# Optimization experiments

Measured on AMD Instinct MI355X. Metric: run time of the kernel, lower is better.

The kernel has to match this reference:

```python
import jax, jax.numpy as jnp
import numpy as np

B, S, C, H, W = 4, 8, 3, 384, 384
K = 5
CK = C * K


def conv1x1(x, w, b):
    # x: [B, Cin, H, W], w: [Cout, Cin], b: [Cout] -> [B, Cout, H, W]
    return jnp.einsum('bchw,oc->bohw', x, w) + b[None, :, None, None]


def mlp(x, w1, b1, w2, b2):
    return conv1x1(jax.nn.relu(conv1x1(x, w1, b1)), w2, b2)


def gaussian_density(x, mu_k, sigma):
    # x: [B,C,H,W], mu_k: [B,K,C,H,W], sigma: [B,K,H,W] -> density [B,K,H,W]
    s2 = sigma * sigma
    dist = jnp.sum((x[:, None] - mu_k) ** 2, axis=2)  # [B,K,H,W]
    return (2.0 * np.pi * s2) ** (-C / 2.0) * jnp.exp(-dist / (2.0 * s2))


def gmm_block(params, x, pi, mu, sigma):
    b = x.shape[0]
    mu_k = mu.reshape(b, K, C, H, W)
    dens = gaussian_density(x, mu_k, sigma)          # [B,K,H,W] (computed once, reused)
    alpha = pi * dens                                 # [B,K,H,W]
    rho = alpha * dens                                # [B,K,H,W]
    pi_new = jax.nn.softmax(mlp(jnp.concatenate([pi, alpha], 1), *params['pi']), axis=1)
    mu_new = jax.nn.sigmoid(mlp(jnp.concatenate([x, mu, rho], 1), *params['mu']))
    sigma_new = jnp.exp(jax.nn.relu(mlp(jnp.concatenate([x, mu_new, rho], 1), *params['sigma'])))
    dens2 = gaussian_density(x, mu_new.reshape(b, K, C, H, W), sigma_new)
    gamma = jax.nn.sigmoid(mlp(pi_new * dens2, *params['gamma']))  # [B,1,H,W]
    return pi_new, mu_new, sigma_new, gamma


def setup_inputs() -> dict:
    key = jax.random.key(0)
    ks = jax.random.split(key, 20)
    frames = jax.random.uniform(ks[0], (B, S, C, H, W), jnp.float32)
    targets = jax.random.uniform(ks[1], (B, S, C, H, W), jnp.float32)
    mu0 = jax.random.randint(ks[2], (B, CK, H, W), 0, 255).astype(jnp.float32) / 255.0
    def wb(k1, k2, cout, cin):
        return (jax.random.normal(k1, (cout, cin), jnp.float32) * 0.1,
                jax.random.normal(k2, (cout,), jnp.float32) * 0.1)
    pi_w1, pi_b1 = wb(ks[3], ks[4], K, 2 * K)
    pi_w2, pi_b2 = wb(ks[5], ks[6], K, K)
    mu_w1, mu_b1 = wb(ks[7], ks[8], CK, C + CK + K)
    mu_w2, mu_b2 = wb(ks[9], ks[10], CK, CK)
    sg_w1, sg_b1 = wb(ks[11], ks[12], K, C + CK + K)
    sg_w2, sg_b2 = wb(ks[13], ks[14], K, K)
    ga_w1, ga_b1 = wb(ks[15], ks[16], K, K)
    ga_w2, ga_b2 = wb(ks[17], ks[18], 1, K)
    return dict(frames=frames, targets=targets, mu0=mu0,
                pi_w1=pi_w1, pi_b1=pi_b1, pi_w2=pi_w2, pi_b2=pi_b2,
                mu_w1=mu_w1, mu_b1=mu_b1, mu_w2=mu_w2, mu_b2=mu_b2,
                sg_w1=sg_w1, sg_b1=sg_b1, sg_w2=sg_w2, sg_b2=sg_b2,
                ga_w1=ga_w1, ga_b1=ga_b1, ga_w2=ga_w2, ga_b2=ga_b2)


def reference(frames, targets, mu0,
              pi_w1, pi_b1, pi_w2, pi_b2,
              mu_w1, mu_b1, mu_w2, mu_b2,
              sg_w1, sg_b1, sg_w2, sg_b2,
              ga_w1, ga_b1, ga_w2, ga_b2):
    params = dict(pi=(pi_w1, pi_b1, pi_w2, pi_b2),
                  mu=(mu_w1, mu_b1, mu_w2, mu_b2),
                  sigma=(sg_w1, sg_b1, sg_w2, sg_b2),
                  gamma=(ga_w1, ga_b1, ga_w2, ga_b2))
    b = frames.shape[0]
    # init_gmm
    pi0 = jnp.ones((b, K, H, W), frames.dtype) / K
    sigma0 = jnp.ones((b, K, H, W), frames.dtype)

    def step(carry, frame):
        pi, mu, sigma = carry
        pi, mu, sigma, gamma = gmm_block(params, frame, pi, mu, sigma)
        return (pi, mu, sigma), gamma

    xs = jnp.moveaxis(frames, 1, 0)  # [S,B,C,H,W]
    _, gammas = jax.lax.scan(step, (pi0, mu0, sigma0), xs)
    return jnp.moveaxis(gammas, 0, 1)  # [B,S,1,H,W]
```

## Files before the change

### kernel.cpp

```cpp
#include <hip/hip_runtime.h>


namespace {

constexpr int Kk = 5;
constexpr int Cc = 3;
constexpr int CKc = 15;
constexpr int Bb = 4;
constexpr int Ss = 8;
constexpr int HWc = 384 * 384;

constexpr int PW1 = 0,   PP1 = 12;
constexpr int PB1 = 60;
constexpr int PW2 = 68,  PP2 = 8;
constexpr int PB2 = 108;
constexpr int MW1 = 116, MP1 = 24;
constexpr int MB1 = 476;
constexpr int MW2 = 492, MP2 = 16;
constexpr int MB2 = 732;
constexpr int SW1 = 748, SP1 = 24;
constexpr int SB1 = 868;
constexpr int SW2 = 876, SP2 = 8;
constexpr int SB2 = 916;
constexpr int GW1 = 924, GP1 = 8;
constexpr int GB1 = 964;
constexpr int GW2 = 972;
constexpr int GB2 = 980;
constexpr int WTOT = 984;

__device__ __forceinline__ float rcpf(float x) { return __builtin_amdgcn_rcpf(x); }
__device__ __forceinline__ float sigm(float x) { return rcpf(1.0f + __expf(-x)); }
__device__ __forceinline__ float relu(float x) { return fmaxf(x, 0.0f); }

__device__ __forceinline__ void stage(float* W, int dst, const float* __restrict__ src,
                                      int rows, int cols, int pitch, int tid) {
    for (int t = tid; t < rows * pitch; t += 256) {
        int r = t / pitch, c = t - r * pitch;
        W[dst + t] = (c < cols) ? src[r * cols + c] : 0.0f;
    }
}

__global__ __launch_bounds__(256) void gmm_seq_kernel(
    const float* __restrict__ frames,
    const float* __restrict__ mu0,
    const float* __restrict__ pw1, const float* __restrict__ pb1,
    const float* __restrict__ pw2, const float* __restrict__ pb2,
    const float* __restrict__ mw1, const float* __restrict__ mb1,
    const float* __restrict__ mw2, const float* __restrict__ mb2,
    const float* __restrict__ sw1, const float* __restrict__ sb1,
    const float* __restrict__ sw2, const float* __restrict__ sb2,
    const float* __restrict__ gw1, const float* __restrict__ gb1,
    const float* __restrict__ gw2, const float* __restrict__ gb2,
    float* __restrict__ out)
{
    __shared__ float sW[WTOT];
    {
        const int t = threadIdx.x;
        stage(sW, PW1, pw1, Kk, 2 * Kk, PP1, t);
        stage(sW, PB1, pb1, 1, Kk, 8, t);
        stage(sW, PW2, pw2, Kk, Kk, PP2, t);
        stage(sW, PB2, pb2, 1, Kk, 8, t);
        stage(sW, MW1, mw1, CKc, 23, MP1, t);
        stage(sW, MB1, mb1, 1, CKc, 16, t);
        stage(sW, MW2, mw2, CKc, CKc, MP2, t);
        stage(sW, MB2, mb2, 1, CKc, 16, t);
        stage(sW, SW1, sw1, Kk, 23, SP1, t);
        stage(sW, SB1, sb1, 1, Kk, 8, t);
        stage(sW, SW2, sw2, Kk, Kk, SP2, t);
        stage(sW, SB2, sb2, 1, Kk, 8, t);
        stage(sW, GW1, gw1, Kk, Kk, GP1, t);
        stage(sW, GB1, gb1, 1, Kk, 8, t);
        stage(sW, GW2, gw2, 1, Kk, 8, t);
        stage(sW, GB2, gb2, 1, 1, 4, t);
    }
    __syncthreads();

    const int tid = blockIdx.x * blockDim.x + threadIdx.x;
    const int b  = tid / HWc;
    const int hw = tid - b * HWc;

    const float C0 = 0.06349363593424097f;

    float pi[Kk], mu[CKc], rinv[Kk];
#pragma unroll
    for (int k = 0; k < Kk; k++) { pi[k] = 0.2f; rinv[k] = 1.0f; }
    {
        const float* mp = mu0 + (size_t)b * CKc * HWc + hw;
#pragma unroll
        for (int j = 0; j < CKc; j++) mu[j] = mp[(size_t)j * HWc];
    }

    const float* fbase = frames + ((size_t)b * Ss * Cc) * HWc + hw;
    float x[Cc];
#pragma unroll
    for (int c = 0; c < Cc; c++) x[c] = fbase[(size_t)c * HWc];

#pragma unroll 1
    for (int s = 0; s < Ss; s++) {
        unsigned woff = 0;
        asm volatile("" : "+v"(woff));
        woff &= ~3u;
#define LW(IDX) sW[woff + (IDX)]

        float xn[Cc];
        if (s + 1 < Ss) {
            const float* fp = fbase + ((size_t)(s + 1) * Cc) * HWc;
#pragma unroll
            for (int c = 0; c < Cc; c++) xn[c] = fp[(size_t)c * HWc];
        }

        float dens[Kk];
#pragma unroll
        for (int k = 0; k < Kk; k++) {
            float inv_s2 = rinv[k] * rinv[k];
            float d0 = x[0] - mu[k * Cc + 0];
            float d1 = x[1] - mu[k * Cc + 1];
            float d2 = x[2] - mu[k * Cc + 2];
            float dist = d0 * d0 + d1 * d1 + d2 * d2;
            float coef = C0 * inv_s2 * rinv[k];
            dens[k] = coef * __expf(-0.5f * dist * inv_s2);
        }

        float alpha[Kk], rho[Kk];
#pragma unroll
        for (int k = 0; k < Kk; k++) { alpha[k] = pi[k] * dens[k]; rho[k] = alpha[k] * dens[k]; }

        float piN[Kk];
        {
            float in[2 * Kk];
#pragma unroll
            for (int k = 0; k < Kk; k++) { in[k] = pi[k]; in[Kk + k] = alpha[k]; }
            float h[Kk];
#pragma unroll
            for (int j = 0; j < Kk; j++) {
                float a = LW(PB1 + j);
#pragma unroll
                for (int i = 0; i < 2 * Kk; i++) a = fmaf(LW(PW1 + j * PP1 + i), in[i], a);
                h[j] = relu(a);
            }
            float o[Kk];
            float m = -1e30f;
#pragma unroll
            for (int j = 0; j < Kk; j++) {
                float a = LW(PB2 + j);
#pragma unroll
                for (int i = 0; i < Kk; i++) a = fmaf(LW(PW2 + j * PP2 + i), h[i], a);
                o[j] = a; m = fmaxf(m, a);
            }
            float sum = 0.0f;
#pragma unroll
            for (int j = 0; j < Kk; j++) { o[j] = __expf(o[j] - m); sum += o[j]; }
            float r = rcpf(sum);
#pragma unroll
            for (int j = 0; j < Kk; j++) piN[j] = o[j] * r;
        }

        float in23[23];
        in23[0] = x[0]; in23[1] = x[1]; in23[2] = x[2];
#pragma unroll
        for (int j = 0; j < CKc; j++) in23[3 + j] = mu[j];
#pragma unroll
        for (int k = 0; k < Kk; k++) in23[18 + k] = rho[k];

        float muN[CKc];
        {
            float h[CKc];
#pragma unroll
            for (int j = 0; j < CKc; j++) {
                float a = LW(MB1 + j);
#pragma unroll
                for (int i = 0; i < 23; i++) a = fmaf(LW(MW1 + j * MP1 + i), in23[i], a);
                h[j] = relu(a);
            }
#pragma unroll
            for (int j = 0; j < CKc; j++) {
                float a = LW(MB2 + j);
#pragma unroll
                for (int i = 0; i < CKc; i++) a = fmaf(LW(MW2 + j * MP2 + i), h[i], a);
                muN[j] = sigm(a);
            }
        }

#pragma unroll
        for (int j = 0; j < CKc; j++) in23[3 + j] = muN[j];
        float rinvN[Kk];
        {
            float h[Kk];
#pragma unroll
            for (int j = 0; j < Kk; j++) {
                float a = LW(SB1 + j);
#pragma unroll
                for (int i = 0; i < 23; i++) a = fmaf(LW(SW1 + j * SP1 + i), in23[i], a);
                h[j] = relu(a);
            }
#pragma unroll
            for (int j = 0; j < Kk; j++) {
                float a = LW(SB2 + j);
#pragma unroll
                for (int i = 0; i < Kk; i++) a = fmaf(LW(SW2 + j * SP2 + i), h[i], a);
                rinvN[j] = __expf(-relu(a));
            }
        }

        float gin[Kk];
#pragma unroll
        for (int k = 0; k < Kk; k++) {
            float inv_s2 = rinvN[k] * rinvN[k];
            float d0 = x[0] - muN[k * Cc + 0];
            float d1 = x[1] - muN[k * Cc + 1];
            float d2 = x[2] - muN[k * Cc + 2];
            float dist = d0 * d0 + d1 * d1 + d2 * d2;
            float coef = C0 * inv_s2 * rinvN[k];
            gin[k] = piN[k] * (coef * __expf(-0.5f * dist * inv_s2));
        }
        {
            float h[Kk];
#pragma unroll
            for (int j = 0; j < Kk; j++) {
                float a = LW(GB1 + j);
#pragma unroll
                for (int i = 0; i < Kk; i++) a = fmaf(LW(GW1 + j * GP1 + i), gin[i], a);
                h[j] = relu(a);
            }
            float go = LW(GB2);
#pragma unroll
            for (int i = 0; i < Kk; i++) go = fmaf(LW(GW2 + i), h[i], go);
            out[(size_t)(b * Ss + s) * HWc + hw] = sigm(go);
        }
#undef LW

#pragma unroll
        for (int k = 0; k < Kk; k++) { pi[k] = piN[k]; rinv[k] = rinvN[k]; }
#pragma unroll
        for (int j = 0; j < CKc; j++) mu[j] = muN[j];
#pragma unroll
        for (int c = 0; c < Cc; c++) x[c] = xn[c];
    }
}

}

extern "C" void kernel_launch(void* const* d_in, const int* in_sizes, int n_in,
                              void* d_out, int out_size, void* d_ws, size_t ws_size,
                              hipStream_t stream) {
    const float* frames = (const float*)d_in[0];
    const float* mu0    = (const float*)d_in[2];
    const float* pw1 = (const float*)d_in[3];
    const float* pb1 = (const float*)d_in[4];
    const float* pw2 = (const float*)d_in[5];
    const float* pb2 = (const float*)d_in[6];
    const float* mw1 = (const float*)d_in[7];
    const float* mb1 = (const float*)d_in[8];
    const float* mw2 = (const float*)d_in[9];
    const float* mb2 = (const float*)d_in[10];
    const float* sw1 = (const float*)d_in[11];
    const float* sb1 = (const float*)d_in[12];
    const float* sw2 = (const float*)d_in[13];
    const float* sb2 = (const float*)d_in[14];
    const float* gw1 = (const float*)d_in[15];
    const float* gb1 = (const float*)d_in[16];
    const float* gw2 = (const float*)d_in[17];
    const float* gb2 = (const float*)d_in[18];
    float* out = (float*)d_out;

    const int total = Bb * HWc;
    const int block = 256;
    const int grid = (total + block - 1) / block;

    gmm_seq_kernel<<<grid, block, 0, stream>>>(
        frames, mu0,
        pw1, pb1, pw2, pb2,
        mw1, mb1, mw2, mb2,
        sw1, sb1, sw2, sb2,
        gw1, gb1, gw2, gb2,
        out);
}
```

Measured before the change: 336.5 us.

## Process two pixels per thread with float2 packed math

New measurement: 315.9 us. 6.1% less time.

```diff
diff --git a/kernel.cpp b/kernel.cpp
--- a/kernel.cpp
+++ b/kernel.cpp
@@ -9,6 +9,9 @@
 constexpr int Bb = 4;
 constexpr int Ss = 8;
 constexpr int HWc = 384 * 384;
+constexpr int HW2 = HWc / 2;
+
+typedef float v2f __attribute__((ext_vector_type(2)));
 
 constexpr int PW1 = 0,   PP1 = 12;
 constexpr int PB1 = 60;
@@ -29,8 +32,15 @@
 constexpr int WTOT = 984;
 
 __device__ __forceinline__ float rcpf(float x) { return __builtin_amdgcn_rcpf(x); }
-__device__ __forceinline__ float sigm(float x) { return rcpf(1.0f + __expf(-x)); }
-__device__ __forceinline__ float relu(float x) { return fmaxf(x, 0.0f); }
+
+__device__ __forceinline__ v2f vsplat(float w) { v2f r = {w, w}; return r; }
+__device__ __forceinline__ v2f vfma(v2f a, v2f b, v2f c) { return __builtin_elementwise_fma(a, b, c); }
+__device__ __forceinline__ v2f wfma(float w, v2f x, v2f c) { return vfma(vsplat(w), x, c); }
+__device__ __forceinline__ v2f vexp(v2f v) { v2f r; r.x = __expf(v.x); r.y = __expf(v.y); return r; }
+__device__ __forceinline__ v2f vrcp(v2f v) { v2f r; r.x = rcpf(v.x); r.y = rcpf(v.y); return r; }
+__device__ __forceinline__ v2f vmax(v2f a, v2f b) { return __builtin_elementwise_max(a, b); }
+__device__ __forceinline__ v2f vrelu(v2f a) { return vmax(a, vsplat(0.0f)); }
+__device__ __forceinline__ v2f vsigm(v2f a) { return vrcp(vsplat(1.0f) + vexp(-a)); }
 
 __device__ __forceinline__ void stage(float* W, int dst, const float* __restrict__ src,
                                       int rows, int cols, int pitch, int tid) {
@@ -75,25 +85,27 @@
     }
     __syncthreads();
 
-    const int tid = blockIdx.x * blockDim.x + threadIdx.x;
-    const int b  = tid / HWc;
-    const int hw = tid - b * HWc;
+    const int t2 = blockIdx.x * blockDim.x + threadIdx.x;
+    const int b   = t2 / HW2;
+    const int rem = t2 - b * HW2;
 
     const float C0 = 0.06349363593424097f;
 
-    float pi[Kk], mu[CKc], rinv[Kk];
-#pragma unroll
-    for (int k = 0; k < Kk; k++) { pi[k] = 0.2f; rinv[k] = 1.0f; }
+    v2f pi[Kk], mu[CKc], rinv[Kk];
+#pragma unroll
+    for (int k = 0; k < Kk; k++) { pi[k] = vsplat(0.2f); rinv[k] = vsplat(1.0f); }
     {
-        const float* mp = mu0 + (size_t)b * CKc * HWc + hw;
-#pragma unroll
-        for (int j = 0; j < CKc; j++) mu[j] = mp[(size_t)j * HWc];
-    }
-
-    const float* fbase = frames + ((size_t)b * Ss * Cc) * HWc + hw;
-    float x[Cc];
-#pragma unroll
-    for (int c = 0; c < Cc; c++) x[c] = fbase[(size_t)c * HWc];
+        const float* mp = mu0 + (size_t)b * CKc * HWc;
+#pragma unroll
+        for (int j = 0; j < CKc; j++)
+            mu[j] = reinterpret_cast<const v2f*>(mp + (size_t)j * HWc)[rem];
+    }
+
+    const float* fbase = frames + ((size_t)b * Ss * Cc) * HWc;
+    v2f x[Cc];
+#pragma unroll
+    for (int c = 0; c < Cc; c++)
+        x[c] = reinterpret_cast<const v2f*>(fbase + (size_t)c * HWc)[rem];
 
 #pragma unroll 1
     for (int s = 0; s < Ss; s++) {
@@ -102,130 +114,129 @@
         woff &= ~3u;
 #define LW(IDX) sW[woff + (IDX)]
 
-        float xn[Cc];
+        v2f xn[Cc];
         if (s + 1 < Ss) {
             const float* fp = fbase + ((size_t)(s + 1) * Cc) * HWc;
 #pragma unroll
-            for (int c = 0; c < Cc; c++) xn[c] = fp[(size_t)c * HWc];
-        }
-
-        float dens[Kk];
+            for (int c = 0; c < Cc; c++)
+                xn[c] = reinterpret_cast<const v2f*>(fp + (size_t)c * HWc)[rem];
+        }
+
+        v2f dens[Kk];
 #pragma unroll
         for (int k = 0; k < Kk; k++) {
-            float inv_s2 = rinv[k] * rinv[k];
-            float d0 = x[0] - mu[k * Cc + 0];
-            float d1 = x[1] - mu[k * Cc + 1];
-            float d2 = x[2] - mu[k * Cc + 2];
-            float dist = d0 * d0 + d1 * d1 + d2 * d2;
-            float coef = C0 * inv_s2 * rinv[k];
-            dens[k] = coef * __expf(-0.5f * dist * inv_s2);
-        }
-
-        float alpha[Kk], rho[Kk];
+            v2f inv_s2 = rinv[k] * rinv[k];
+            v2f d0 = x[0] - mu[k * Cc + 0];
+            v2f d1 = x[1] - mu[k * Cc + 1];
+            v2f d2 = x[2] - mu[k * Cc + 2];
+            v2f dist = vfma(d0, d0, vfma(d1, d1, d2 * d2));
+            v2f coef = vsplat(C0) * inv_s2 * rinv[k];
+            dens[k] = coef * vexp(vsplat(-0.5f) * dist * inv_s2);
+        }
+
+        v2f alpha[Kk], rho[Kk];
 #pragma unroll
         for (int k = 0; k < Kk; k++) { alpha[k] = pi[k] * dens[k]; rho[k] = alpha[k] * dens[k]; }
 
-        float piN[Kk];
-        {
-            float in[2 * Kk];
-#pragma unroll
-            for (int k = 0; k < Kk; k++) { in[k] = pi[k]; in[Kk + k] = alpha[k]; }
-            float h[Kk];
-#pragma unroll
-            for (int j = 0; j < Kk; j++) {
-                float a = LW(PB1 + j);
-#pragma unroll
-                for (int i = 0; i < 2 * Kk; i++) a = fmaf(LW(PW1 + j * PP1 + i), in[i], a);
-                h[j] = relu(a);
-            }
-            float o[Kk];
-            float m = -1e30f;
-#pragma unroll
-            for (int j = 0; j < Kk; j++) {
-                float a = LW(PB2 + j);
-#pragma unroll
-                for (int i = 0; i < Kk; i++) a = fmaf(LW(PW2 + j * PP2 + i), h[i], a);
-                o[j] = a; m = fmaxf(m, a);
-            }
-            float sum = 0.0f;
-#pragma unroll
-            for (int j = 0; j < Kk; j++) { o[j] = __expf(o[j] - m); sum += o[j]; }
-            float r = rcpf(sum);
+        v2f piN[Kk];
+        {
+            v2f h[Kk];
+#pragma unroll
+            for (int j = 0; j < Kk; j++) {
+                v2f a = vsplat(LW(PB1 + j));
+#pragma unroll
+                for (int i = 0; i < Kk; i++) a = wfma(LW(PW1 + j * PP1 + i), pi[i], a);
+#pragma unroll
+                for (int i = 0; i < Kk; i++) a = wfma(LW(PW1 + j * PP1 + Kk + i), alpha[i], a);
+                h[j] = vrelu(a);
+            }
+            v2f o[Kk];
+            v2f m = vsplat(-1e30f);
+#pragma unroll
+            for (int j = 0; j < Kk; j++) {
+                v2f a = vsplat(LW(PB2 + j));
+#pragma unroll
+                for (int i = 0; i < Kk; i++) a = wfma(LW(PW2 + j * PP2 + i), h[i], a);
+                o[j] = a; m = vmax(m, a);
+            }
+            v2f sum = vsplat(0.0f);
+#pragma unroll
+            for (int j = 0; j < Kk; j++) { o[j] = vexp(o[j] - m); sum = sum + o[j]; }
+            v2f r = vrcp(sum);
 #pragma unroll
             for (int j = 0; j < Kk; j++) piN[j] = o[j] * r;
         }
 
-        float in23[23];
-        in23[0] = x[0]; in23[1] = x[1]; in23[2] = x[2];
-#pragma unroll
-        for (int j = 0; j < CKc; j++) in23[3 + j] = mu[j];
-#pragma unroll
-        for (int k = 0; k < Kk; k++) in23[18 + k] = rho[k];
-
-        float muN[CKc];
-        {
-            float h[CKc];
+        v2f muN[CKc];
+        {
+            v2f h[CKc];
 #pragma unroll
             for (int j = 0; j < CKc; j++) {
-                float a = LW(MB1 + j);
-#pragma unroll
-                for (int i = 0; i < 23; i++) a = fmaf(LW(MW1 + j * MP1 + i), in23[i], a);
-                h[j] = relu(a);
+                v2f a = vsplat(LW(MB1 + j));
+#pragma unroll
+                for (int i = 0; i < Cc; i++)  a = wfma(LW(MW1 + j * MP1 + i), x[i], a);
+#pragma unroll
+                for (int i = 0; i < CKc; i++) a = wfma(LW(MW1 + j * MP1 + 3 + i), mu[i], a);
+#pragma unroll
+                for (int i = 0; i < Kk; i++)  a = wfma(LW(MW1 + j * MP1 + 18 + i), rho[i], a);
+                h[j] = vrelu(a);
             }
 #pragma unroll
             for (int j = 0; j < CKc; j++) {
-                float a = LW(MB2 + j);
-#pragma unroll
-                for (int i = 0; i < CKc; i++) a = fmaf(LW(MW2 + j * MP2 + i), h[i], a);
-                muN[j] = sigm(a);
-            }
-        }
-
-#pragma unroll
-        for (int j = 0; j < CKc; j++) in23[3 + j] = muN[j];
-        float rinvN[Kk];
-        {
-            float h[Kk];
-#pragma unroll
-            for (int j = 0; j < Kk; j++) {
-                float a = LW(SB1 + j);
-#pragma unroll
-                for (int i = 0; i < 23; i++) a = fmaf(LW(SW1 + j * SP1 + i), in23[i], a);
-                h[j] = relu(a);
-            }
-#pragma unroll
-            for (int j = 0; j < Kk; j++) {
-                float a = LW(SB2 + j);
-#pragma unroll
-                for (int i = 0; i < Kk; i++) a = fmaf(LW(SW2 + j * SP2 + i), h[i], a);
-                rinvN[j] = __expf(-relu(a));
-            }
-        }
-
-        float gin[Kk];
+                v2f a = vsplat(LW(MB2 + j));
+#pragma unroll
+                for (int i = 0; i < CKc; i++) a = wfma(LW(MW2 + j * MP2 + i), h[i], a);
+                muN[j] = vsigm(a);
+            }
+        }
+
+        v2f rinvN[Kk];
+        {
+            v2f h[Kk];
+#pragma unroll
+            for (int j = 0; j < Kk; j++) {
+                v2f a = vsplat(LW(SB1 + j));
+#pragma unroll
+                for (int i = 0; i < Cc; i++)  a = wfma(LW(SW1 + j * SP1 + i), x[i], a);
+#pragma unroll
+                for (int i = 0; i < CKc; i++) a = wfma(LW(SW1 + j * SP1 + 3 + i), muN[i], a);
+#pragma unroll
+                for (int i = 0; i < Kk; i++)  a = wfma(LW(SW1 + j * SP1 + 18 + i), rho[i], a);
+                h[j] = vrelu(a);
+            }
+#pragma unroll
+            for (int j = 0; j < Kk; j++) {
+                v2f a = vsplat(LW(SB2 + j));
+#pragma unroll
+                for (int i = 0; i < Kk; i++) a = wfma(LW(SW2 + j * SP2 + i), h[i], a);
+                rinvN[j] = vexp(-vrelu(a));
+            }
+        }
+
+        v2f gin[Kk];
 #pragma unroll
         for (int k = 0; k < Kk; k++) {
-            float inv_s2 = rinvN[k] * rinvN[k];
-            float d0 = x[0] - muN[k * Cc + 0];
-            float d1 = x[1] - muN[k * Cc + 1];
-            float d2 = x[2] - muN[k * Cc + 2];
-            float dist = d0 * d0 + d1 * d1 + d2 * d2;
-            float coef = C0 * inv_s2 * rinvN[k];
-            gin[k] = piN[k] * (coef * __expf(-0.5f * dist * inv_s2));
-        }
-        {
-            float h[Kk];
-#pragma unroll
-            for (int j = 0; j < Kk; j++) {
-                float a = LW(GB1 + j);
-#pragma unroll
-                for (int i = 0; i < Kk; i++) a = fmaf(LW(GW1 + j * GP1 + i), gin[i], a);
-                h[j] = relu(a);
-            }
-            float go = LW(GB2);
-#pragma unroll
-            for (int i = 0; i < Kk; i++) go = fmaf(LW(GW2 + i), h[i], go);
-            out[(size_t)(b * Ss + s) * HWc + hw] = sigm(go);
+            v2f inv_s2 = rinvN[k] * rinvN[k];
+            v2f d0 = x[0] - muN[k * Cc + 0];
+            v2f d1 = x[1] - muN[k * Cc + 1];
+            v2f d2 = x[2] - muN[k * Cc + 2];
+            v2f dist = vfma(d0, d0, vfma(d1, d1, d2 * d2));
+            v2f coef = vsplat(C0) * inv_s2 * rinvN[k];
+            gin[k] = piN[k] * (coef * vexp(vsplat(-0.5f) * dist * inv_s2));
+        }
+        {
+            v2f h[Kk];
+#pragma unroll
+            for (int j = 0; j < Kk; j++) {
+                v2f a = vsplat(LW(GB1 + j));
+#pragma unroll
+                for (int i = 0; i < Kk; i++) a = wfma(LW(GW1 + j * GP1 + i), gin[i], a);
+                h[j] = vrelu(a);
+            }
+            v2f go = vsplat(LW(GB2));
+#pragma unroll
+            for (int i = 0; i < Kk; i++) go = wfma(LW(GW2 + i), h[i], go);
+            reinterpret_cast<v2f*>(out + (size_t)(b * Ss + s) * HWc)[rem] = vsigm(go);
         }
 #undef LW
 
@@ -263,9 +274,9 @@
     const float* gb2 = (const float*)d_in[18];
     float* out = (float*)d_out;
 
-    const int total = Bb * HWc;
+    const int total2 = Bb * HW2;
     const int block = 256;
-    const int grid = (total + block - 1) / block;
+    const int grid = (total2 + block - 1) / block;
 
     gmm_seq_kernel<<<grid, block, 0, stream>>>(
         frames, mu0,
```
